# Kernel optimization log

Hardware: AMD Instinct MI355X
Metric: run time of the kernel (lower is better)

Reference implementation:

```python
import jax, jax.numpy as jnp
import numpy as np

NC = 4        # num_components
HEADS = 24
DH = 64
D = HEADS * DH  # 1536
EPS = 1e-8


def setup_inputs() -> dict:
    key = jax.random.key(0)
    ks = jax.random.split(key, 7)
    btc, S, E = 4, 4096, 154
    w = lambda k: jax.random.normal(k, (D, D), jnp.float32) * 0.02
    return {
        "hidden_states": jax.random.normal(ks[0], (btc, S, D), jnp.float32),
        "encoder_hidden_states": jax.random.normal(ks[1], (btc, E, D), jnp.float32),
        "temperature": jnp.ones((1,), jnp.float32),
        "Wq": w(ks[2]),
        "Wk": w(ks[3]),
        "Wv": w(ks[4]),
        "Wo": w(ks[5]),
        "bo": jnp.zeros((D,), jnp.float32),
        "pad_length": 154,
    }


def reference(hidden_states, encoder_hidden_states, temperature, Wq, Wk, Wv, Wo, bo, pad_length):
    btc, S, d = hidden_states.shape          # batch*components, latent seq, hidden
    E = encoder_hidden_states.shape[1]       # encoder seq (== pad_length)
    b = btc // NC
    scale = DH ** -0.5
    residual = hidden_states

    def heads(x, L):  # [btc, L, D] -> [btc, H, L, dh]
        return x.reshape(btc, L, HEADS, DH).transpose(0, 2, 1, 3)

    q = heads(hidden_states @ Wq.T, S)
    k = heads(encoder_hidden_states @ Wk.T, E)
    v = heads(encoder_hidden_states @ Wv.T, E)

    # pad tokens are zeros projected through the same k/v weights (no bias -> zeros)
    pad_h = jnp.zeros((btc, pad_length, d), hidden_states.dtype)
    k_pad = heads(pad_h @ Wk.T, pad_length)
    v_pad = heads(pad_h @ Wv.T, pad_length)

    scores = jnp.einsum('bhsd,bhed->bhse', q, k) / (temperature[0] + EPS)
    scores_pad = jnp.einsum('bhsd,bhpd->bhsp', q, k_pad) * scale

    # cross-component softmax over dim 0
    scores = scores.reshape(NC, b, HEADS, S, E)
    scores_pad = scores_pad.reshape(NC, b, HEADS, S, pad_length)
    w = jax.nn.softmax(scores, axis=0)
    w_pad = jax.nn.softmax(scores_pad, axis=0) * (NC / pad_length) * (1.0 - w)

    weights = jnp.concatenate(
        [w.reshape(btc, HEADS, S, E), w_pad.reshape(btc, HEADS, S, pad_length)],
        axis=-1)                              # [btc, H, S, E+pad]
    v_cat = jnp.concatenate([v, v_pad], axis=2)  # [btc, H, E+pad, dh]

    out = jnp.einsum('bhse,bhed->bhsd', weights, v_cat)
    out = out.transpose(0, 2, 1, 3).reshape(btc, S, d)
    out = out @ Wo.T + bo
    return out + residual
```

## Files before the change

### kernel.cpp

```cpp
#include <hip/hip_runtime.h>

typedef __attribute__((ext_vector_type(8))) short short8;
typedef __attribute__((ext_vector_type(4))) float f32x4;
typedef __attribute__((ext_vector_type(4))) unsigned short us4;
typedef __attribute__((ext_vector_type(4))) float float4v;

#define GLB_PTR(p) ((const __attribute__((address_space(1))) void*)(p))
#define LDS_PTR(p) ((__attribute__((address_space(3))) void*)(p))

__device__ __forceinline__ unsigned short f2bf(float f) {
  unsigned int u = __float_as_uint(f);
  u += 0x7FFF + ((u >> 16) & 1);
  return (unsigned short)(u >> 16);
}

__global__ void cvt_all(const float* __restrict__ i0, const float* __restrict__ i1,
                        const float* __restrict__ i2, const float* __restrict__ i3,
                        const float* __restrict__ i4, const float* __restrict__ i5,
                        unsigned short* __restrict__ o0, unsigned short* __restrict__ o1,
                        unsigned short* __restrict__ o2, unsigned short* __restrict__ o3,
                        unsigned short* __restrict__ o4, unsigned short* __restrict__ o5) {
  const float* in; unsigned short* out; int n4;
  switch (blockIdx.y) {
    case 0:  in = i0; out = o0; n4 = 16384 * 1536 / 4; break;
    case 1:  in = i1; out = o1; n4 = 616 * 1536 / 4;   break;
    case 2:  in = i2; out = o2; n4 = 1536 * 1536 / 4;  break;
    case 3:  in = i3; out = o3; n4 = 1536 * 1536 / 4;  break;
    case 4:  in = i4; out = o4; n4 = 1536 * 1536 / 4;  break;
    default: in = i5; out = o5; n4 = 1536 * 1536 / 4;  break;
  }
  int i = blockIdx.x * blockDim.x + threadIdx.x;
  int stride = gridDim.x * blockDim.x;
  for (; i < n4; i += stride) {
    float4v v = *(const float4v*)(in + (size_t)i * 4);
    us4 o;
    o[0] = f2bf(v[0]); o[1] = f2bf(v[1]); o[2] = f2bf(v[2]); o[3] = f2bf(v[3]);
    *(us4*)(out + (size_t)i * 4) = o;
  }
}

template<int MODE>
__device__ __forceinline__ void gemm_big_body(
    const unsigned short* __restrict__ A,
    const unsigned short* __restrict__ B,
    unsigned short* __restrict__ Cb,
    float* __restrict__ Cf,
    const float* __restrict__ bias,
    const float* __restrict__ resid,
    unsigned short* smem, int bid, int tid) {
  constexpr int K = 1536, N = 1536, BK = 32, NKT = K / BK;
  unsigned short* As = smem;
  unsigned short* Bs = smem + 2 * 8192;

  const int xcd = bid & 7, idx = bid >> 3;
  const int m0 = (xcd * 8 + idx / 12) * 256;
  const int n0 = (idx % 12) * 128;

  const int w = tid >> 6, l = tid & 63, lr = l & 15, lg = l >> 4;
  const int wr = w >> 1, wc = w & 1;
  const int ga = lg ^ (lr & 3);

  const int srow = w * 16 + (l >> 2);
  const int sg = (l & 3) ^ ((l >> 2) & 3);
  const unsigned short* aSrc = A + (size_t)(m0 + srow) * K + sg * 8;
  const unsigned short* bSrc = B + (size_t)(n0 + srow) * K + sg * 8;

  f32x4 acc[4][4] = {};

  auto stage = [&](int buf, int kt) {
    const int k0 = kt * BK;
    unsigned short* AsW = As + buf * 8192 + w * 512;
    unsigned short* BsW = Bs + buf * 4096 + w * 512;
    __builtin_amdgcn_global_load_lds(GLB_PTR(aSrc + k0),                    LDS_PTR(AsW),        16, 0, 0);
    __builtin_amdgcn_global_load_lds(GLB_PTR(aSrc + (size_t)128 * K + k0),  LDS_PTR(AsW + 4096), 16, 0, 0);
    __builtin_amdgcn_global_load_lds(GLB_PTR(bSrc + k0),                    LDS_PTR(BsW),        16, 0, 0);
  };

  auto loadfrags = [&](int buf, short8* af, short8* bfv) {
    const unsigned short* Asb = As + buf * 8192;
    const unsigned short* Bsb = Bs + buf * 4096;
#pragma unroll
    for (int i = 0; i < 4; ++i)
      af[i] = *(const short8*)(Asb + (wr * 64 + i * 16 + lr) * 32 + ga * 8);
#pragma unroll
    for (int j = 0; j < 4; ++j)
      bfv[j] = *(const short8*)(Bsb + (wc * 64 + j * 16 + lr) * 32 + ga * 8);
  };

  auto mfma_all = [&](short8* af, short8* bfv) {
#pragma unroll
    for (int i = 0; i < 4; ++i)
#pragma unroll
      for (int j = 0; j < 4; ++j)
        acc[i][j] = __builtin_amdgcn_mfma_f32_16x16x32_bf16(af[i], bfv[j], acc[i][j], 0, 0, 0);
  };

  stage(0, 0); stage(1, 1);

  for (int kt = 0; kt < NKT; ++kt) {
    if (kt < NKT - 1) asm volatile("s_waitcnt vmcnt(3)" ::: "memory");
    else              asm volatile("s_waitcnt vmcnt(0)" ::: "memory");
    __builtin_amdgcn_s_barrier();
    __builtin_amdgcn_sched_barrier(0);
    short8 af[4], bfv[4];
    loadfrags(kt & 1, af, bfv);
    asm volatile("s_waitcnt lgkmcnt(0)" ::: "memory");
    __builtin_amdgcn_sched_barrier(0);
    __builtin_amdgcn_s_barrier();
    __builtin_amdgcn_sched_barrier(0);
    if (kt + 2 < NKT) stage(kt & 1, kt + 2);
    __builtin_amdgcn_s_setprio(1);
    mfma_all(af, bfv);
    __builtin_amdgcn_s_setprio(0);
  }

#pragma unroll
  for (int i = 0; i < 4; ++i) {
    const int rb = m0 + wr * 64 + i * 16 + lg * 4;
#pragma unroll
    for (int j = 0; j < 4; ++j) {
      const int col = n0 + wc * 64 + j * 16 + lr;
#pragma unroll
      for (int r = 0; r < 4; ++r) {
        size_t o = (size_t)(rb + r) * N + col;
        if (MODE == 0) Cb[o] = f2bf(acc[i][j][r]);
        else           Cf[o] = acc[i][j][r] + bias[col] + resid[o];
      }
    }
  }
}

__device__ __forceinline__ void gemm_kv_body(
    const unsigned short* __restrict__ A,
    const unsigned short* __restrict__ Bk,
    const unsigned short* __restrict__ Bv,
    unsigned short* __restrict__ Ck,
    unsigned short* __restrict__ Vt,
    unsigned short* smem, int by, int tid) {
  constexpr int K = 1536, N = 1536, Mc = 615;
  unsigned short* As = smem;
  unsigned short* Bs = smem + 4096;
  const int bx = by % 5, yy = by / 5;
  const unsigned short* B = yy < 12 ? Bk : Bv;
  const int m0 = bx * 128, n0 = (yy % 12) * 128;
  const bool act = tid < 256;
  const int t = tid;
  const int w = t >> 6, l = t & 63, lr = l & 15, lg = l >> 4;
  const int wr = w >> 1, wc = w & 1;
  const int srow = t >> 2, scol = (t & 3) * 8;

  f32x4 acc[4][4] = {};
  unsigned short* AsW = As + w * 512;
  unsigned short* BsW = Bs + w * 512;
  long ar0 = m0 + srow;       if (ar0 > Mc) ar0 = Mc;
  long ar1 = m0 + srow + 64;  if (ar1 > Mc) ar1 = Mc;

  for (int k0 = 0; k0 < K; k0 += 32) {
    if (act) {
      __builtin_amdgcn_global_load_lds(GLB_PTR(A + ar0 * (long)K + k0 + scol), LDS_PTR(AsW),        16, 0, 0);
      __builtin_amdgcn_global_load_lds(GLB_PTR(A + ar1 * (long)K + k0 + scol), LDS_PTR(AsW + 2048), 16, 0, 0);
      __builtin_amdgcn_global_load_lds(GLB_PTR(B + (long)(n0 + srow) * K + k0 + scol),      LDS_PTR(BsW),        16, 0, 0);
      __builtin_amdgcn_global_load_lds(GLB_PTR(B + (long)(n0 + srow + 64) * K + k0 + scol), LDS_PTR(BsW + 2048), 16, 0, 0);
    }
    __syncthreads();
    if (act) {
      short8 af[4], bfv[4];
#pragma unroll
      for (int i = 0; i < 4; ++i) {
        af[i]  = *(const short8*)(As + (wr * 64 + i * 16 + lr) * 32 + lg * 8);
        bfv[i] = *(const short8*)(Bs + (wc * 64 + i * 16 + lr) * 32 + lg * 8);
      }
#pragma unroll
      for (int i = 0; i < 4; ++i)
#pragma unroll
        for (int j = 0; j < 4; ++j)
          acc[i][j] = __builtin_amdgcn_mfma_f32_16x16x32_bf16(af[i], bfv[j], acc[i][j], 0, 0, 0);
    }
    __syncthreads();
  }

  if (!act) return;
  if (yy < 12) {
#pragma unroll
    for (int i = 0; i < 4; ++i) {
      int rb = m0 + wr * 64 + i * 16 + lg * 4;
#pragma unroll
      for (int j = 0; j < 4; ++j) {
        int col = n0 + wc * 64 + j * 16 + lr;
#pragma unroll
        for (int r = 0; r < 4; ++r)
          Ck[(long)(rb + r) * N + col] = f2bf(acc[i][j][r]);
      }
    }
  } else {
#pragma unroll
    for (int i = 0; i < 4; ++i) {
      int rb = m0 + wr * 64 + i * 16 + lg * 4;
#pragma unroll
      for (int j = 0; j < 4; ++j) {
        int col = n0 + wc * 64 + j * 16 + lr;
        int hh = col >> 6, dd = col & 63;
#pragma unroll
        for (int r = 0; r < 4; ++r) {
          int m = rb + r;
          if (m < 616) {
            int c = (unsigned)m / 154u;
            int e = m - c * 154;
            Vt[((long)((c * 24 + hh) * 64 + dd)) * 160 + e] = f2bf(acc[i][j][r]);
          }
        }
      }
    }
  }
}

__global__ __launch_bounds__(512, 4) void gemm_q_kv(
    const unsigned short* __restrict__ HSb, const unsigned short* __restrict__ Wqb,
    unsigned short* __restrict__ Qb,
    const unsigned short* __restrict__ EHSb, const unsigned short* __restrict__ Wkb,
    const unsigned short* __restrict__ Wvb,
    unsigned short* __restrict__ Ck, unsigned short* __restrict__ Vt) {
  __shared__ unsigned short smem[24576];
  if (blockIdx.x < 768)
    gemm_big_body<0>(HSb, Wqb, Qb, nullptr, nullptr, nullptr, smem, blockIdx.x, threadIdx.x);
  else
    gemm_kv_body(EHSb, Wkb, Wvb, Ck, Vt, smem, blockIdx.x - 768, threadIdx.x);
}

__global__ __launch_bounds__(512, 4) void gemm_o(
    const unsigned short* __restrict__ Ob, const unsigned short* __restrict__ Wob,
    float* __restrict__ Cf, const float* __restrict__ bias, const float* __restrict__ resid) {
  __shared__ unsigned short smem[24576];
  gemm_big_body<1>(Ob, Wob, nullptr, Cf, bias, resid, smem, blockIdx.x, threadIdx.x);
}

__global__ __launch_bounds__(256) void attn_kernel(
    const unsigned short* __restrict__ Qb,
    const unsigned short* __restrict__ Kb,
    const unsigned short* __restrict__ Vt,
    const float* __restrict__ temp,
    unsigned short* __restrict__ Ob) {
  __shared__ unsigned short P[4][4][16][160];
  const int h = blockIdx.y, sb = blockIdx.x;
  const int t = threadIdx.x, w = t >> 6, l = t & 63, lr = l & 15, lg = l >> 4;
  const int s0 = sb * 64 + w * 16;
  const float sc = 1.0f / (temp[0] + 1e-8f);

  short8 qf[4][2];
#pragma unroll
  for (int c = 0; c < 4; ++c)
#pragma unroll
    for (int kt = 0; kt < 2; ++kt)
      qf[c][kt] = *(const short8*)(Qb + (long)(c * 4096 + s0 + lr) * 1536 + h * 64 + kt * 32 + lg * 8);

  short8 kA[4][2], kB[4][2];
  auto loadK = [&](int et, short8 (&k)[4][2]) {
#pragma unroll
    for (int c = 0; c < 4; ++c)
#pragma unroll
      for (int kt = 0; kt < 2; ++kt)
        k[c][kt] = *(const short8*)(Kb + (long)(c * 154 + et * 16 + lr) * 1536 + h * 64 + kt * 32 + lg * 8);
  };

  auto qk_step = [&](int et, short8 (&kc)[4][2], short8 (&kn)[4][2], bool pre) {
    if (pre) loadK(et + 1, kn);
    f32x4 sa[4] = {};
#pragma unroll
    for (int c = 0; c < 4; ++c)
#pragma unroll
      for (int kt = 0; kt < 2; ++kt)
        sa[c] = __builtin_amdgcn_mfma_f32_16x16x32_bf16(kc[c][kt], qf[c][kt], sa[c], 0, 0, 0);
    float wv[4][4];
#pragma unroll
    for (int r = 0; r < 4; ++r) {
      float e0 = __expf(sa[0][r] * sc), e1 = __expf(sa[1][r] * sc);
      float e2 = __expf(sa[2][r] * sc), e3 = __expf(sa[3][r] * sc);
      float inv = 1.0f / (e0 + e1 + e2 + e3);
      wv[0][r] = e0 * inv; wv[1][r] = e1 * inv; wv[2][r] = e2 * inv; wv[3][r] = e3 * inv;
    }
#pragma unroll
    for (int c = 0; c < 4; ++c) {
      us4 pk;
#pragma unroll
      for (int r = 0; r < 4; ++r)
        pk[r] = (et * 16 + lg * 4 + r < 154) ? f2bf(wv[c][r]) : (unsigned short)0;
      *(us4*)&P[w][c][lr][et * 16 + lg * 4] = pk;
    }
  };

  loadK(0, kA);
#pragma unroll
  for (int et = 0; et < 10; et += 2) {
    qk_step(et,     kA, kB, true);
    qk_step(et + 1, kB, kA, et + 1 < 9);
  }
  __syncthreads();

  short8 vA[4], vB[4];
  auto loadV = [&](int c, int ks, short8 (&v)[4]) {
#pragma unroll
    for (int nt = 0; nt < 4; ++nt)
      v[nt] = *(const short8*)(Vt + (long)((c * 24 + h) * 64 + nt * 16 + lr) * 160 + ks * 32 + lg * 8);
  };

  f32x4 o[4][4] = {};
  loadV(0, 0, vA);
#pragma unroll
  for (int p = 0; p < 10; ++p) {
    const int i0 = 2 * p, i1 = 2 * p + 1;
    const int c0 = i0 / 5, k0 = i0 % 5;
    const int c1 = i1 / 5, k1 = i1 % 5;
    loadV(c1, k1, vB);
    short8 pf0 = *(const short8*)&P[w][c0][lr][k0 * 32 + lg * 8];
#pragma unroll
    for (int nt = 0; nt < 4; ++nt)
      o[c0][nt] = __builtin_amdgcn_mfma_f32_16x16x32_bf16(pf0, vA[nt], o[c0][nt], 0, 0, 0);
    if (p < 9) loadV((i1 + 1) / 5, (i1 + 1) % 5, vA);
    short8 pf1 = *(const short8*)&P[w][c1][lr][k1 * 32 + lg * 8];
#pragma unroll
    for (int nt = 0; nt < 4; ++nt)
      o[c1][nt] = __builtin_amdgcn_mfma_f32_16x16x32_bf16(pf1, vB[nt], o[c1][nt], 0, 0, 0);
  }

#pragma unroll
  for (int c = 0; c < 4; ++c)
#pragma unroll
    for (int nt = 0; nt < 4; ++nt)
#pragma unroll
      for (int r = 0; r < 4; ++r)
        Ob[(long)(c * 4096 + s0 + lg * 4 + r) * 1536 + h * 64 + nt * 16 + lr] = f2bf(o[c][nt][r]);
}

extern "C" void kernel_launch(void* const* d_in, const int* in_sizes, int n_in,
                              void* d_out, int out_size, void* d_ws, size_t ws_size,
                              hipStream_t stream) {
  (void)in_sizes; (void)n_in; (void)out_size; (void)ws_size;
  const float* HS  = (const float*)d_in[0];
  const float* EHS = (const float*)d_in[1];
  const float* TMP = (const float*)d_in[2];
  const float* Wq  = (const float*)d_in[3];
  const float* Wk  = (const float*)d_in[4];
  const float* Wv  = (const float*)d_in[5];
  const float* Wo  = (const float*)d_in[6];
  const float* bo  = (const float*)d_in[7];

  char* ws = (char*)d_ws;
  size_t off = 0;
  unsigned short* HSb  = (unsigned short*)(ws + off); off += (size_t)16384 * 1536 * 2;
  unsigned short* Ob   = HSb;
  unsigned short* EHSb = (unsigned short*)(ws + off); off += (size_t)616 * 1536 * 2;
  unsigned short* Wqb  = (unsigned short*)(ws + off); off += (size_t)1536 * 1536 * 2;
  unsigned short* Wkb  = (unsigned short*)(ws + off); off += (size_t)1536 * 1536 * 2;
  unsigned short* Wvb  = (unsigned short*)(ws + off); off += (size_t)1536 * 1536 * 2;
  unsigned short* Wob  = (unsigned short*)(ws + off); off += (size_t)1536 * 1536 * 2;
  unsigned short* Kb   = (unsigned short*)(ws + off); off += (size_t)640 * 1536 * 2;
  unsigned short* Vt   = (unsigned short*)(ws + off); off += (size_t)4 * 24 * 64 * 160 * 2;
  unsigned short* Qb   = (unsigned short*)d_out;

  cvt_all<<<dim3(1024, 6), 256, 0, stream>>>(HS, EHS, Wq, Wk, Wv, Wo,
                                             HSb, EHSb, Wqb, Wkb, Wvb, Wob);

  gemm_q_kv<<<888, 512, 0, stream>>>(HSb, Wqb, Qb, EHSb, Wkb, Wvb, Kb, Vt);

  attn_kernel<<<dim3(64, 24), 256, 0, stream>>>(Qb, Kb, Vt, TMP, Ob);

  gemm_o<<<768, 512, 0, stream>>>(Ob, Wob, (float*)d_out, bo, HS);
}
```

Measured before the change: 357.9 us.

## Flatten conversion grid, drop attention barrier, stage output through LDS

After: 353.6 us, median of 2. About the same (-1.2%).

```diff
diff --git a/kernel.cpp b/kernel.cpp
--- a/kernel.cpp
+++ b/kernel.cpp
@@ -20,22 +20,24 @@
                         unsigned short* __restrict__ o0, unsigned short* __restrict__ o1,
                         unsigned short* __restrict__ o2, unsigned short* __restrict__ o3,
                         unsigned short* __restrict__ o4, unsigned short* __restrict__ o5) {
-  const float* in; unsigned short* out; int n4;
-  switch (blockIdx.y) {
-    case 0:  in = i0; out = o0; n4 = 16384 * 1536 / 4; break;
-    case 1:  in = i1; out = o1; n4 = 616 * 1536 / 4;   break;
-    case 2:  in = i2; out = o2; n4 = 1536 * 1536 / 4;  break;
-    case 3:  in = i3; out = o3; n4 = 1536 * 1536 / 4;  break;
-    case 4:  in = i4; out = o4; n4 = 1536 * 1536 / 4;  break;
-    default: in = i5; out = o5; n4 = 1536 * 1536 / 4;  break;
-  }
+  constexpr int N0 = 16384 * 1536 / 4, N1 = 616 * 1536 / 4, NW = 1536 * 1536 / 4;
+  constexpr int TOT = N0 + N1 + 4 * NW;
   int i = blockIdx.x * blockDim.x + threadIdx.x;
-  int stride = gridDim.x * blockDim.x;
-  for (; i < n4; i += stride) {
-    float4v v = *(const float4v*)(in + (size_t)i * 4);
+  const int stride = gridDim.x * blockDim.x;
+  for (; i < TOT; i += stride) {
+    const float* in; unsigned short* out; int j = i;
+    if (j < N0)              { in = i0; out = o0; }
+    else if ((j -= N0) < N1) { in = i1; out = o1; }
+    else {
+      j -= N1;
+      const int t = j / NW; j -= t * NW;
+      in  = t == 0 ? i2 : t == 1 ? i3 : t == 2 ? i4 : i5;
+      out = t == 0 ? o2 : t == 1 ? o3 : t == 2 ? o4 : o5;
+    }
+    float4v v = *(const float4v*)(in + (size_t)j * 4);
     us4 o;
     o[0] = f2bf(v[0]); o[1] = f2bf(v[1]); o[2] = f2bf(v[2]); o[3] = f2bf(v[3]);
-    *(us4*)(out + (size_t)i * 4) = o;
+    *(us4*)(out + (size_t)j * 4) = o;
   }
 }
 
@@ -294,7 +296,8 @@
     qk_step(et,     kA, kB, true);
     qk_step(et + 1, kB, kA, et + 1 < 9);
   }
-  __syncthreads();
+  asm volatile("s_waitcnt lgkmcnt(0)" ::: "memory");
+  __builtin_amdgcn_sched_barrier(0);
 
   short8 vA[4], vB[4];
   auto loadV = [&](int c, int ks, short8 (&v)[4]) {
@@ -322,13 +325,24 @@
       o[c1][nt] = __builtin_amdgcn_mfma_f32_16x16x32_bf16(pf1, vB[nt], o[c1][nt], 0, 0, 0);
   }
 
-#pragma unroll
-  for (int c = 0; c < 4; ++c)
+  unsigned short* OS = &P[w][0][0][0];
+#pragma unroll
+  for (int c = 0; c < 4; ++c) {
 #pragma unroll
     for (int nt = 0; nt < 4; ++nt)
 #pragma unroll
       for (int r = 0; r < 4; ++r)
-        Ob[(long)(c * 4096 + s0 + lg * 4 + r) * 1536 + h * 64 + nt * 16 + lr] = f2bf(o[c][nt][r]);
+        OS[(lg * 4 + r) * 64 + nt * 16 + lr] = f2bf(o[c][nt][r]);
+    asm volatile("s_waitcnt lgkmcnt(0)" ::: "memory");
+    __builtin_amdgcn_sched_barrier(0);
+#pragma unroll
+    for (int p = 0; p < 2; ++p) {
+      const int flat = p * 512 + l * 8;
+      const int row = flat >> 6, col = flat & 63;
+      short8 v = *(const short8*)(OS + flat);
+      *(short8*)(Ob + (long)(c * 4096 + s0 + row) * 1536 + h * 64 + col) = v;
+    }
+  }
 }
 
 extern "C" void kernel_launch(void* const* d_in, const int* in_sizes, int n_in,
@@ -357,8 +371,8 @@
   unsigned short* Vt   = (unsigned short*)(ws + off); off += (size_t)4 * 24 * 64 * 160 * 2;
   unsigned short* Qb   = (unsigned short*)d_out;
 
-  cvt_all<<<dim3(1024, 6), 256, 0, stream>>>(HS, EHS, Wq, Wk, Wv, Wo,
-                                             HSb, EHSb, Wqb, Wkb, Wvb, Wob);
+  cvt_all<<<2048, 256, 0, stream>>>(HS, EHS, Wq, Wk, Wv, Wo,
+                                    HSb, EHSb, Wqb, Wkb, Wvb, Wob);
 
   gemm_q_kv<<<888, 512, 0, stream>>>(HSb, Wqb, Qb, EHSb, Wkb, Wvb, Kb, Vt);
 
```
